# Kernel tuning notes

Measured on AMD Instinct MI355X. Metric: run time of the kernel, lower is better.

The kernel has to match this reference:

```python
import jax, jax.numpy as jnp
import numpy as np

INPUT_DIM = 128
HIDDEN_DIM = 128
N_PATIENTS = 200000
N_CONDITIONS = 5000
N_EDGES = 1000000
IN_FEAT = INPUT_DIM * 2 + 1  # 257


def _linear_params(key, fan_in, fan_out):
    # torch nn.Linear default init: U(-1/sqrt(fan_in), 1/sqrt(fan_in))
    kw, kb = jax.random.split(key)
    bound = 1.0 / np.sqrt(fan_in)
    W = jax.random.uniform(kw, (fan_in, fan_out), jnp.float32, -bound, bound)
    b = jax.random.uniform(kb, (fan_out,), jnp.float32, -bound, bound)
    return W, b


def setup_inputs() -> dict:
    key = jax.random.key(0)
    ks = jax.random.split(key, 8)
    patient_embeds = jax.random.normal(ks[0], (N_PATIENTS, INPUT_DIM), jnp.float32)
    condition_embeds = jax.random.normal(ks[1], (N_CONDITIONS, INPUT_DIM), jnp.float32)
    src_idx = jax.random.randint(ks[2], (N_EDGES,), 0, N_PATIENTS)
    dst_idx = jax.random.randint(ks[3], (N_EDGES,), 0, N_CONDITIONS)
    edge_index = jnp.stack([src_idx, dst_idx], axis=0)
    tte = jax.random.uniform(ks[4], (N_EDGES,), jnp.float32)
    W1, b1 = _linear_params(ks[5], IN_FEAT, HIDDEN_DIM)
    W2, b2 = _linear_params(ks[6], HIDDEN_DIM, HIDDEN_DIM)
    k7, k8 = jax.random.split(ks[7])
    Wo, bo = _linear_params(k7, HIDDEN_DIM, 1)
    Wr, br = _linear_params(k8, IN_FEAT, HIDDEN_DIM)
    return {
        "patient_embeds": patient_embeds,
        "condition_embeds": condition_embeds,
        "edge_index": edge_index,
        "tte": tte,
        "W1": W1, "b1": b1,
        "W2": W2, "b2": b2,
        "Wo": Wo, "bo": bo,
        "Wr": Wr, "br": br,
    }


def reference(patient_embeds, condition_embeds, edge_index, tte,
              W1, b1, W2, b2, Wo, bo, Wr, br):
    src = patient_embeds[edge_index[0]]        # [E, D]
    dst = condition_embeds[edge_index[1]]      # [E, D]
    x = jnp.concatenate([src, dst, tte[:, None]], axis=1)  # [E, 2D+1]
    h1 = jax.nn.relu(x @ W1 + b1)              # [E, H]
    res = x @ Wr + br                          # [E, H]
    h2 = jax.nn.relu(h1 @ W2 + b2 + res)       # [E, H]
    return (h2 @ Wo + bo).reshape(-1)          # [E]
```

## Files before the change

kernel.cpp:

```cpp
#include <hip/hip_runtime.h>
#include <hip/hip_bf16.h>

using u16   = unsigned short;
using u16x4 = __attribute__((ext_vector_type(4))) unsigned short;
using u16x8 = __attribute__((ext_vector_type(8))) unsigned short;
using s16x8 = __attribute__((ext_vector_type(8))) short;
using f32x4 = __attribute__((ext_vector_type(4))) float;

#define KPAD 136
#define XP   136
#define OP   264
#define EB   64

__device__ __forceinline__ float bf2f(u16 u){
  unsigned int x = ((unsigned int)u) << 16;
  float f; __builtin_memcpy(&f, &x, 4); return f;
}
__device__ __forceinline__ u16 f2bf(float f){
  __hip_bfloat16 h = __float2bfloat16(f);
  u16 u; __builtin_memcpy(&u, &h, 2); return u;
}
__device__ __forceinline__ f32x4 mfma16(s16x8 a, s16x8 b, f32x4 c){
  return __builtin_amdgcn_mfma_f32_16x16x32_bf16(a, b, c, 0, 0, 0);
}

__global__ __launch_bounds__(256) void prep_kernel(
    const float* __restrict__ W1, const float* __restrict__ W2,
    const float* __restrict__ Wo, const float* __restrict__ Wr,
    const float* __restrict__ b1, const float* __restrict__ b2,
    const float* __restrict__ br,
    u16* __restrict__ WF, u16* __restrict__ W2T, float* __restrict__ params)
{
  const int tid = blockIdx.x*256 + threadIdx.x;
  const int nth = gridDim.x*256;
  for (int id = tid; id < 131072; id += nth){
    const int j    = id & 7;
    const int lane = (id >> 3) & 63;
    const int pair = (id >> 9) & 1;
    const int ks   = (id >> 10) & 3;
    const int nb   = (id >> 12) & 15;
    const int h    = (id >> 16) & 1;
    const int k = ks*32 + (lane >> 4)*8 + j;
    const int n = nb*16 + (lane & 15);
    const float v = ((n < 128) ? W1 : Wr)[(h*128 + k)*128 + (n & 127)];
    const u16 hi = f2bf(v);
    WF[id] = pair ? f2bf(v - bf2f(hi)) : hi;
  }
  for (int id = tid; id < 128*128; id += nth){
    const int k = id >> 7, n = id & 127;
    W2T[n*KPAD + k] = f2bf(W2[k*128 + n]);
  }
  for (int id = tid; id < 128; id += nth){
    params[id]       = W1[256*128 + id];
    params[128 + id] = Wr[256*128 + id];
    params[256 + id] = Wo[id];
    params[384 + id]       = b1[id];
    params[384 + 128 + id] = br[id] + b2[id];
  }
}

__global__ __launch_bounds__(1024, 4) void mm_kernel(
    const float* __restrict__ emb, int nrows, int ntiles,
    const u16* __restrict__ WFh,
    const float* __restrict__ bias,
    u16* __restrict__ outbuf)
{
  __shared__ __align__(16) char smem_raw[2*128*XP*2];
  u16* xhi = (u16*)smem_raw;
  u16* xlo = xhi + 128*XP;
  u16* sO  = (u16*)smem_raw;
  const int t = threadIdx.x;
  const int l = t & 63, w = t >> 6;
  const int lrow = l & 15, lq = l >> 4;
  s16x8 wf0h, wf0l, wf1h, wf1l, wf2h, wf2l, wf3h, wf3l;
  {
    const u16* base = WFh + w*4096 + l*8;
    wf0h = *(const s16x8*)(base +    0); wf0l = *(const s16x8*)(base +  512);
    wf1h = *(const s16x8*)(base + 1024); wf1l = *(const s16x8*)(base + 1536);
    wf2h = *(const s16x8*)(base + 2048); wf2l = *(const s16x8*)(base + 2560);
    wf3h = *(const s16x8*)(base + 3072); wf3l = *(const s16x8*)(base + 3584);
  }
  float bv[4] = {0.f, 0.f, 0.f, 0.f};
  if (bias){
#pragma unroll
    for (int r = 0; r < 4; ++r) bv[r] = bias[w*16 + lq*4 + r];
  }
  for (int tile = blockIdx.x; tile < ntiles; tile += gridDim.x){
    const int row0 = tile*128;
    __syncthreads();
#pragma unroll
    for (int i = 0; i < 4; ++i){
      const int f4 = i*1024 + t;
      const int r = f4 >> 5, kc = f4 & 31;
      int grow = row0 + r; if (grow >= nrows) grow = nrows - 1;
      const float4 v = *(const float4*)(emb + (size_t)grow*128 + kc*4);
      const float vv[4] = {v.x, v.y, v.z, v.w};
      u16x4 h4, l4;
#pragma unroll
      for (int q = 0; q < 4; ++q){
        const u16 hi = f2bf(vv[q]);
        h4[q] = hi;
        l4[q] = f2bf(vv[q] - bf2f(hi));
      }
      *(u16x4*)(xhi + r*XP + kc*4) = h4;
      *(u16x4*)(xlo + r*XP + kc*4) = l4;
    }
    __syncthreads();
    f32x4 acc[8];
#pragma unroll
    for (int mb = 0; mb < 8; ++mb) acc[mb] = (f32x4){0.f,0.f,0.f,0.f};
#pragma unroll
    for (int mb = 0; mb < 8; ++mb){
      const int mro = (mb*16 + lrow)*XP + lq*8;
      const s16x8 xh0 = *(const s16x8*)(xhi + mro +  0);
      const s16x8 xl0 = *(const s16x8*)(xlo + mro +  0);
      const s16x8 xh1 = *(const s16x8*)(xhi + mro + 32);
      const s16x8 xl1 = *(const s16x8*)(xlo + mro + 32);
      const s16x8 xh2 = *(const s16x8*)(xhi + mro + 64);
      const s16x8 xl2 = *(const s16x8*)(xlo + mro + 64);
      const s16x8 xh3 = *(const s16x8*)(xhi + mro + 96);
      const s16x8 xl3 = *(const s16x8*)(xlo + mro + 96);
      acc[mb] = mfma16(wf0h, xh0, acc[mb]);
      acc[mb] = mfma16(wf0l, xh0, acc[mb]);
      acc[mb] = mfma16(wf0h, xl0, acc[mb]);
      acc[mb] = mfma16(wf1h, xh1, acc[mb]);
      acc[mb] = mfma16(wf1l, xh1, acc[mb]);
      acc[mb] = mfma16(wf1h, xl1, acc[mb]);
      acc[mb] = mfma16(wf2h, xh2, acc[mb]);
      acc[mb] = mfma16(wf2l, xh2, acc[mb]);
      acc[mb] = mfma16(wf2h, xl2, acc[mb]);
      acc[mb] = mfma16(wf3h, xh3, acc[mb]);
      acc[mb] = mfma16(wf3l, xh3, acc[mb]);
      acc[mb] = mfma16(wf3h, xl3, acc[mb]);
    }
    __syncthreads();
#pragma unroll
    for (int mb = 0; mb < 8; ++mb){
      const int m = mb*16 + lrow;
      u16x4 o;
#pragma unroll
      for (int r = 0; r < 4; ++r) o[r] = f2bf(acc[mb][r] + bv[r]);
      *(u16x4*)(sO + m*OP + w*16 + lq*4) = o;
    }
    __syncthreads();
#pragma unroll
    for (int i = 0; i < 4; ++i){
      const int idx = i*1024 + t;
      const int m = idx >> 5, c = idx & 31;
      const int grow = row0 + m;
      if (grow < nrows){
        const u16x8 v = *(const u16x8*)(sO + m*OP + c*8);
        *(u16x8*)(outbuf + (size_t)grow*256 + c*8) = v;
      }
    }
  }
}

__global__ __launch_bounds__(512, 4) void edge_kernel(
    const int* __restrict__ ei, const float* __restrict__ tte,
    const u16* __restrict__ PP, const u16* __restrict__ CC,
    const u16* __restrict__ W2T, const float* __restrict__ params,
    const float* __restrict__ bo_p, float* __restrict__ out, int E, int ntiles)
{
  __shared__ u16 sW2T[128*KPAD];
  __shared__ u16 sA[EB*KPAD];
  __shared__ u16 sR[EB*KPAD];
  __shared__ float sw1t[128], swrt[128], sWo[128];
  __shared__ int ssrc[EB], sdst[EB];
  __shared__ float stte[EB];
  __shared__ float souts[4][EB];
  const int t = threadIdx.x;
  {
    const u16x8* g = (const u16x8*)W2T;
    u16x8* s = (u16x8*)sW2T;
    for (int i = t; i < 128*KPAD/8; i += 512) s[i] = g[i];
  }
  if (t < 128){ sw1t[t] = params[t]; swrt[t] = params[128+t]; sWo[t] = params[256+t]; }
  const float bo = bo_p[0];
  const int l = t & 63, w = t >> 6;
  const int lrow = l & 15, lk = l >> 4;
  const int rh = w & 1, ch = w >> 1;

  for (int tile = blockIdx.x; tile < ntiles; tile += gridDim.x){
    const int e0 = tile * EB;
    if (t < EB){
      int e = e0 + t; if (e >= E) e = E - 1;
      ssrc[t] = ei[e]; sdst[t] = ei[E + e]; stte[t] = tte[e];
    }
    __syncthreads();
    u16x8 pv[4], cv[4];
#pragma unroll
    for (int i = 0; i < 4; ++i){
      const int id = i*512 + t;
      const int e = id >> 5, c = id & 31;
      pv[i] = *(const u16x8*)(PP + (size_t)ssrc[e]*256 + c*8);
      cv[i] = *(const u16x8*)(CC + (size_t)sdst[e]*256 + c*8);
    }
#pragma unroll
    for (int i = 0; i < 4; ++i){
      const int id = i*512 + t;
      const int e = id >> 5, c = id & 31;
      const float tt = stte[e];
      const int jj = (c & 15)*8;
      const float* wt = (c < 16) ? sw1t : swrt;
      u16x8 o;
#pragma unroll
      for (int q = 0; q < 8; ++q){
        float v = bf2f(pv[i][q]) + bf2f(cv[i][q]) + tt * wt[jj+q];
        if (c < 16) v = fmaxf(v, 0.f);
        o[q] = f2bf(v);
      }
      u16* dst = (c < 16) ? (sA + e*KPAD + jj) : (sR + e*KPAD + jj);
      *(u16x8*)dst = o;
    }
    __syncthreads();
    f32x4 acc[2][2];
#pragma unroll
    for (int mb = 0; mb < 2; ++mb)
#pragma unroll
      for (int nb = 0; nb < 2; ++nb) acc[mb][nb] = (f32x4){0.f,0.f,0.f,0.f};
#pragma unroll
    for (int ks = 0; ks < 4; ++ks){
      const int koff = ks*32 + lk*8;
      const s16x8 a0 = *(const s16x8*)(sA + (rh*32 + lrow)*KPAD + koff);
      const s16x8 a1 = *(const s16x8*)(sA + (rh*32 + 16 + lrow)*KPAD + koff);
      const s16x8 b0 = *(const s16x8*)(sW2T + (ch*32 + lrow)*KPAD + koff);
      const s16x8 b1 = *(const s16x8*)(sW2T + (ch*32 + 16 + lrow)*KPAD + koff);
      acc[0][0] = mfma16(a0, b0, acc[0][0]);
      acc[0][1] = mfma16(a0, b1, acc[0][1]);
      acc[1][0] = mfma16(a1, b0, acc[1][0]);
      acc[1][1] = mfma16(a1, b1, acc[1][1]);
    }
    float p[2][4] = {{0.f,0.f,0.f,0.f},{0.f,0.f,0.f,0.f}};
#pragma unroll
    for (int nb = 0; nb < 2; ++nb){
      const int col = ch*32 + nb*16 + lrow;
      const float wo = sWo[col];
#pragma unroll
      for (int mb = 0; mb < 2; ++mb){
#pragma unroll
        for (int r = 0; r < 4; ++r){
          const int row = rh*32 + mb*16 + lk*4 + r;
          float h2 = acc[mb][nb][r] + bf2f(sR[row*KPAD + col]);
          h2 = fmaxf(h2, 0.f);
          p[mb][r] += h2 * wo;
        }
      }
    }
#pragma unroll
    for (int off = 1; off < 16; off <<= 1){
#pragma unroll
      for (int mb = 0; mb < 2; ++mb)
#pragma unroll
        for (int r = 0; r < 4; ++r)
          p[mb][r] += __shfl_xor(p[mb][r], off, 64);
    }
    if (lrow == 0){
#pragma unroll
      for (int mb = 0; mb < 2; ++mb)
#pragma unroll
        for (int r = 0; r < 4; ++r)
          souts[ch][rh*32 + mb*16 + lk*4 + r] = p[mb][r];
    }
    __syncthreads();
    if (t < EB && e0 + t < E)
      out[e0 + t] = souts[0][t] + souts[1][t] + souts[2][t] + souts[3][t] + bo;
  }
}

__global__ __launch_bounds__(256) void fallback_kernel(
    const float* __restrict__ pe, const float* __restrict__ ce,
    const int* __restrict__ ei, const float* __restrict__ tte,
    const float* __restrict__ W1, const float* __restrict__ b1,
    const float* __restrict__ W2, const float* __restrict__ b2,
    const float* __restrict__ Wo, const float* __restrict__ bo,
    const float* __restrict__ Wr, const float* __restrict__ br,
    float* __restrict__ out, int E)
{
  __shared__ float sh1[4][128];
  const int w = threadIdx.x >> 6, l = threadIdx.x & 63;
  const int e_raw = blockIdx.x*4 + w;
  const int e = e_raw < E ? e_raw : E-1;
  const int s = ei[e], d = ei[E + e];
  const float tt = tte[e];
  const float* xs = pe + (size_t)s*128;
  const float* xd = ce + (size_t)d*128;
  const float x0 = xs[l], x1 = xs[64+l], x2 = xd[l], x3 = xd[64+l];
  float h1a = b1[l], h1b = b1[64+l];
  float ra = br[l], rb = br[64+l];
  for (int k = 0; k < 256; ++k){
    const float xv = (k < 64) ? x0 : (k < 128) ? x1 : (k < 192) ? x2 : x3;
    const float xk = __shfl(xv, k & 63, 64);
    h1a += xk * W1[k*128 + l];
    h1b += xk * W1[k*128 + 64 + l];
    ra  += xk * Wr[k*128 + l];
    rb  += xk * Wr[k*128 + 64 + l];
  }
  h1a += tt * W1[256*128 + l];  h1b += tt * W1[256*128 + 64 + l];
  ra  += tt * Wr[256*128 + l];  rb  += tt * Wr[256*128 + 64 + l];
  sh1[w][l] = fmaxf(h1a, 0.f);
  sh1[w][64+l] = fmaxf(h1b, 0.f);
  __syncthreads();
  float h2a = b2[l] + ra, h2b = b2[64+l] + rb;
  for (int k = 0; k < 128; ++k){
    const float hk = sh1[w][k];
    h2a += hk * W2[k*128 + l];
    h2b += hk * W2[k*128 + 64 + l];
  }
  float sum = fmaxf(h2a,0.f)*Wo[l] + fmaxf(h2b,0.f)*Wo[64+l];
  for (int off = 1; off < 64; off <<= 1) sum += __shfl_xor(sum, off, 64);
  if (l == 0 && e_raw < E) out[e_raw] = sum + bo[0];
}

extern "C" void kernel_launch(void* const* d_in, const int* in_sizes, int n_in,
                              void* d_out, int out_size, void* d_ws, size_t ws_size,
                              hipStream_t stream)
{
  const float* pe  = (const float*)d_in[0];
  const float* ce  = (const float*)d_in[1];
  const int*   ei  = (const int*)d_in[2];
  const float* tte = (const float*)d_in[3];
  const float* W1  = (const float*)d_in[4];
  const float* b1  = (const float*)d_in[5];
  const float* W2  = (const float*)d_in[6];
  const float* b2  = (const float*)d_in[7];
  const float* Wo  = (const float*)d_in[8];
  const float* bo  = (const float*)d_in[9];
  const float* Wr  = (const float*)d_in[10];
  const float* br  = (const float*)d_in[11];
  float* out = (float*)d_out;
  const int E = in_sizes[3];
  const int npat  = in_sizes[0] / 128;
  const int ncond = in_sizes[1] / 128;

  char* ws = (char*)d_ws;
  const size_t sz_PP  = (size_t)npat  * 256 * 2;
  const size_t sz_CC  = (size_t)ncond * 256 * 2;
  const size_t sz_WF  = (size_t)131072 * 2;
  const size_t sz_W2T = (size_t)128 * KPAD * 2;
  const size_t off_PP = 0;
  const size_t off_CC = off_PP + sz_PP;
  const size_t off_WF = off_CC + sz_CC;
  const size_t off_W2T = off_WF + sz_WF;
  const size_t off_params = off_W2T + sz_W2T;
  const size_t ws_needed = off_params + 640*4;

  if (ws_size >= ws_needed){
    u16* PP     = (u16*)(ws + off_PP);
    u16* CCb    = (u16*)(ws + off_CC);
    u16* WF     = (u16*)(ws + off_WF);
    u16* W2T    = (u16*)(ws + off_W2T);
    float* params = (float*)(ws + off_params);
    prep_kernel<<<64, 256, 0, stream>>>(W1, W2, Wo, Wr, b1, b2, br, WF, W2T, params);
    const int ptiles = (npat + 127)/128;
    mm_kernel<<<512, 1024, 0, stream>>>(pe, npat, ptiles, WF, nullptr, PP);
    const int ctiles = (ncond + 127)/128;
    mm_kernel<<<ctiles, 1024, 0, stream>>>(ce, ncond, ctiles, WF + 65536, params + 384, CCb);
    const int etiles = (E + EB - 1)/EB;
    edge_kernel<<<512, 512, 0, stream>>>(ei, tte, PP, CCb, W2T, params, bo, out, E, etiles);
  } else {
    fallback_kernel<<<(E + 3)/4, 256, 0, stream>>>(pe, ce, ei, tte, W1, b1, W2, b2, Wo, bo, Wr, br, out, E);
  }
}
```

Baseline: 381.8 us.

## Prefetch next edge tile gathers, keep W2 fragments in registers, shrink mm tiles

```diff
diff --git a/kernel.cpp b/kernel.cpp
--- a/kernel.cpp
+++ b/kernel.cpp
@@ -12,6 +12,8 @@
 #define OP   264
 #define EB   64
 
+#define BARRIER() asm volatile("s_waitcnt lgkmcnt(0)\n\ts_barrier" ::: "memory")
+
 __device__ __forceinline__ float bf2f(u16 u){
   unsigned int x = ((unsigned int)u) << 16;
   float f; __builtin_memcpy(&f, &x, 4); return f;
@@ -29,7 +31,7 @@
     const float* __restrict__ Wo, const float* __restrict__ Wr,
     const float* __restrict__ b1, const float* __restrict__ b2,
     const float* __restrict__ br,
-    u16* __restrict__ WF, u16* __restrict__ W2T, float* __restrict__ params)
+    u16* __restrict__ WF, u16* __restrict__ WF2, float* __restrict__ params)
 {
   const int tid = blockIdx.x*256 + threadIdx.x;
   const int nth = gridDim.x*256;
@@ -46,9 +48,14 @@
     const u16 hi = f2bf(v);
     WF[id] = pair ? f2bf(v - bf2f(hi)) : hi;
   }
-  for (int id = tid; id < 128*128; id += nth){
-    const int k = id >> 7, n = id & 127;
-    W2T[n*KPAD + k] = f2bf(W2[k*128 + n]);
+  for (int id = tid; id < 16384; id += nth){
+    const int j    = id & 7;
+    const int lane = (id >> 3) & 63;
+    const int ks   = (id >> 9) & 3;
+    const int nb   = (id >> 11) & 7;
+    const int k = ks*32 + (lane >> 4)*8 + j;
+    const int n = nb*16 + (lane & 15);
+    WF2[id] = f2bf(W2[k*128 + n]);
   }
   for (int id = tid; id < 128; id += nth){
     params[id]       = W1[256*128 + id];
@@ -59,38 +66,42 @@
   }
 }
 
-__global__ __launch_bounds__(1024, 4) void mm_kernel(
+__global__ __launch_bounds__(512, 8) void mm_kernel(
     const float* __restrict__ emb, int nrows, int ntiles,
-    const u16* __restrict__ WFh,
-    const float* __restrict__ bias,
+    const u16* __restrict__ WFh, const float* __restrict__ bias,
     u16* __restrict__ outbuf)
 {
-  __shared__ __align__(16) char smem_raw[2*128*XP*2];
+  __shared__ __align__(16) char smem_raw[64*XP*2*2];
   u16* xhi = (u16*)smem_raw;
-  u16* xlo = xhi + 128*XP;
+  u16* xlo = xhi + 64*XP;
   u16* sO  = (u16*)smem_raw;
   const int t = threadIdx.x;
   const int l = t & 63, w = t >> 6;
   const int lrow = l & 15, lq = l >> 4;
-  s16x8 wf0h, wf0l, wf1h, wf1l, wf2h, wf2l, wf3h, wf3l;
-  {
-    const u16* base = WFh + w*4096 + l*8;
-    wf0h = *(const s16x8*)(base +    0); wf0l = *(const s16x8*)(base +  512);
-    wf1h = *(const s16x8*)(base + 1024); wf1l = *(const s16x8*)(base + 1536);
-    wf2h = *(const s16x8*)(base + 2048); wf2l = *(const s16x8*)(base + 2560);
-    wf3h = *(const s16x8*)(base + 3072); wf3l = *(const s16x8*)(base + 3584);
-  }
-  float bv[4] = {0.f, 0.f, 0.f, 0.f};
+  s16x8 wf[2][4][2];
+#pragma unroll
+  for (int nbh = 0; nbh < 2; ++nbh)
+#pragma unroll
+    for (int ks = 0; ks < 4; ++ks){
+      const int nb = w + nbh*8;
+      const u16* base = WFh + (size_t)((nb*4 + ks)*2)*512 + l*8;
+      wf[nbh][ks][0] = *(const s16x8*)(base);
+      wf[nbh][ks][1] = *(const s16x8*)(base + 512);
+    }
+  float bv[2][4] = {{0.f,0.f,0.f,0.f},{0.f,0.f,0.f,0.f}};
   if (bias){
 #pragma unroll
-    for (int r = 0; r < 4; ++r) bv[r] = bias[w*16 + lq*4 + r];
+    for (int nbh = 0; nbh < 2; ++nbh)
+#pragma unroll
+      for (int r = 0; r < 4; ++r)
+        bv[nbh][r] = bias[(w + nbh*8)*16 + lq*4 + r];
   }
   for (int tile = blockIdx.x; tile < ntiles; tile += gridDim.x){
-    const int row0 = tile*128;
-    __syncthreads();
-#pragma unroll
-    for (int i = 0; i < 4; ++i){
-      const int f4 = i*1024 + t;
+    const int row0 = tile*64;
+    BARRIER();
+#pragma unroll
+    for (int i = 0; i < 4; ++i){
+      const int f4 = i*512 + t;
       const int r = f4 >> 5, kc = f4 & 31;
       int grow = row0 + r; if (grow >= nrows) grow = nrows - 1;
       const float4 v = *(const float4*)(emb + (size_t)grow*128 + kc*4);
@@ -105,47 +116,42 @@
       *(u16x4*)(xhi + r*XP + kc*4) = h4;
       *(u16x4*)(xlo + r*XP + kc*4) = l4;
     }
-    __syncthreads();
-    f32x4 acc[8];
-#pragma unroll
-    for (int mb = 0; mb < 8; ++mb) acc[mb] = (f32x4){0.f,0.f,0.f,0.f};
-#pragma unroll
-    for (int mb = 0; mb < 8; ++mb){
+    BARRIER();
+    f32x4 acc[2][4];
+#pragma unroll
+    for (int a = 0; a < 2; ++a)
+#pragma unroll
+      for (int b = 0; b < 4; ++b) acc[a][b] = (f32x4){0.f,0.f,0.f,0.f};
+#pragma unroll
+    for (int mb = 0; mb < 4; ++mb){
       const int mro = (mb*16 + lrow)*XP + lq*8;
-      const s16x8 xh0 = *(const s16x8*)(xhi + mro +  0);
-      const s16x8 xl0 = *(const s16x8*)(xlo + mro +  0);
-      const s16x8 xh1 = *(const s16x8*)(xhi + mro + 32);
-      const s16x8 xl1 = *(const s16x8*)(xlo + mro + 32);
-      const s16x8 xh2 = *(const s16x8*)(xhi + mro + 64);
-      const s16x8 xl2 = *(const s16x8*)(xlo + mro + 64);
-      const s16x8 xh3 = *(const s16x8*)(xhi + mro + 96);
-      const s16x8 xl3 = *(const s16x8*)(xlo + mro + 96);
-      acc[mb] = mfma16(wf0h, xh0, acc[mb]);
-      acc[mb] = mfma16(wf0l, xh0, acc[mb]);
-      acc[mb] = mfma16(wf0h, xl0, acc[mb]);
-      acc[mb] = mfma16(wf1h, xh1, acc[mb]);
-      acc[mb] = mfma16(wf1l, xh1, acc[mb]);
-      acc[mb] = mfma16(wf1h, xl1, acc[mb]);
-      acc[mb] = mfma16(wf2h, xh2, acc[mb]);
-      acc[mb] = mfma16(wf2l, xh2, acc[mb]);
-      acc[mb] = mfma16(wf2h, xl2, acc[mb]);
-      acc[mb] = mfma16(wf3h, xh3, acc[mb]);
-      acc[mb] = mfma16(wf3l, xh3, acc[mb]);
-      acc[mb] = mfma16(wf3h, xl3, acc[mb]);
-    }
-    __syncthreads();
-#pragma unroll
-    for (int mb = 0; mb < 8; ++mb){
-      const int m = mb*16 + lrow;
-      u16x4 o;
-#pragma unroll
-      for (int r = 0; r < 4; ++r) o[r] = f2bf(acc[mb][r] + bv[r]);
-      *(u16x4*)(sO + m*OP + w*16 + lq*4) = o;
-    }
-    __syncthreads();
-#pragma unroll
-    for (int i = 0; i < 4; ++i){
-      const int idx = i*1024 + t;
+#pragma unroll
+      for (int ks = 0; ks < 4; ++ks){
+        const s16x8 xh = *(const s16x8*)(xhi + mro + ks*32);
+        const s16x8 xl = *(const s16x8*)(xlo + mro + ks*32);
+#pragma unroll
+        for (int nbh = 0; nbh < 2; ++nbh){
+          acc[nbh][mb] = mfma16(wf[nbh][ks][0], xh, acc[nbh][mb]);
+          acc[nbh][mb] = mfma16(wf[nbh][ks][1], xh, acc[nbh][mb]);
+          acc[nbh][mb] = mfma16(wf[nbh][ks][0], xl, acc[nbh][mb]);
+        }
+      }
+    }
+    BARRIER();
+#pragma unroll
+    for (int nbh = 0; nbh < 2; ++nbh)
+#pragma unroll
+      for (int mb = 0; mb < 4; ++mb){
+        const int m = mb*16 + lrow;
+        u16x4 o;
+#pragma unroll
+        for (int r = 0; r < 4; ++r) o[r] = f2bf(acc[nbh][mb][r] + bv[nbh][r]);
+        *(u16x4*)(sO + m*OP + (w + nbh*8)*16 + lq*4) = o;
+      }
+    BARRIER();
+#pragma unroll
+    for (int i = 0; i < 4; ++i){
+      const int idx = i*512 + t;
       const int m = idx >> 5, c = idx & 31;
       const int grow = row0 + m;
       if (grow < nrows){
@@ -156,115 +162,136 @@
   }
 }
 
-__global__ __launch_bounds__(512, 4) void edge_kernel(
+__global__ __launch_bounds__(512, 8) void edge_kernel(
     const int* __restrict__ ei, const float* __restrict__ tte,
     const u16* __restrict__ PP, const u16* __restrict__ CC,
-    const u16* __restrict__ W2T, const float* __restrict__ params,
+    const u16* __restrict__ WF2, const float* __restrict__ params,
     const float* __restrict__ bo_p, float* __restrict__ out, int E, int ntiles)
 {
-  __shared__ u16 sW2T[128*KPAD];
   __shared__ u16 sA[EB*KPAD];
   __shared__ u16 sR[EB*KPAD];
-  __shared__ float sw1t[128], swrt[128], sWo[128];
-  __shared__ int ssrc[EB], sdst[EB];
-  __shared__ float stte[EB];
   __shared__ float souts[4][EB];
   const int t = threadIdx.x;
-  {
-    const u16x8* g = (const u16x8*)W2T;
-    u16x8* s = (u16x8*)sW2T;
-    for (int i = t; i < 128*KPAD/8; i += 512) s[i] = g[i];
-  }
-  if (t < 128){ sw1t[t] = params[t]; swrt[t] = params[128+t]; sWo[t] = params[256+t]; }
-  const float bo = bo_p[0];
   const int l = t & 63, w = t >> 6;
   const int lrow = l & 15, lk = l >> 4;
   const int rh = w & 1, ch = w >> 1;
-
-  for (int tile = blockIdx.x; tile < ntiles; tile += gridDim.x){
-    const int e0 = tile * EB;
-    if (t < EB){
-      int e = e0 + t; if (e >= E) e = E - 1;
-      ssrc[t] = ei[e]; sdst[t] = ei[E + e]; stte[t] = tte[e];
-    }
-    __syncthreads();
-    u16x8 pv[4], cv[4];
-#pragma unroll
-    for (int i = 0; i < 4; ++i){
-      const int id = i*512 + t;
-      const int e = id >> 5, c = id & 31;
-      pv[i] = *(const u16x8*)(PP + (size_t)ssrc[e]*256 + c*8);
-      cv[i] = *(const u16x8*)(CC + (size_t)sdst[e]*256 + c*8);
-    }
-#pragma unroll
-    for (int i = 0; i < 4; ++i){
-      const int id = i*512 + t;
-      const int e = id >> 5, c = id & 31;
-      const float tt = stte[e];
-      const int jj = (c & 15)*8;
-      const float* wt = (c < 16) ? sw1t : swrt;
+  const int gid = t >> 5, gl = t & 31;
+  const float bo = bo_p[0];
+  s16x8 wf2[2][4];
+#pragma unroll
+  for (int nb = 0; nb < 2; ++nb)
+#pragma unroll
+    for (int ks = 0; ks < 4; ++ks)
+      wf2[nb][ks] = *(const s16x8*)(WF2 + (size_t)(((ch*2 + nb)*4 + ks)*64 + l)*8);
+  float wt[8];
+  {
+    const float* base = params + ((gl < 16) ? 0 : 128) + (gl & 15)*8;
+#pragma unroll
+    for (int q = 0; q < 8; ++q) wt[q] = base[q];
+  }
+  float wo[2][4];
+#pragma unroll
+  for (int nb = 0; nb < 2; ++nb){
+    const float4 v = *(const float4*)(params + 256 + ch*32 + nb*16 + lk*4);
+    wo[nb][0] = v.x; wo[nb][1] = v.y; wo[nb][2] = v.z; wo[nb][3] = v.w;
+  }
+
+  int tile = blockIdx.x;
+  if (tile >= ntiles) return;
+  float ctt[4];
+  u16x8 cpv[4], ccv[4];
+  {
+    int cs[4], cd[4];
+#pragma unroll
+    for (int i = 0; i < 4; ++i){
+      int e = tile*EB + i*16 + gid; if (e >= E) e = E - 1;
+      cs[i] = ei[e]; cd[i] = ei[E + e]; ctt[i] = tte[e];
+    }
+#pragma unroll
+    for (int i = 0; i < 4; ++i){
+      cpv[i] = *(const u16x8*)(PP + (size_t)cs[i]*256 + gl*8);
+      ccv[i] = *(const u16x8*)(CC + (size_t)cd[i]*256 + gl*8);
+    }
+  }
+
+  for (; tile < ntiles; tile += gridDim.x){
+    const int ntile = tile + gridDim.x;
+    int nxs[4], nxd[4]; float ntt[4];
+#pragma unroll
+    for (int i = 0; i < 4; ++i){
+      int e = ntile*EB + i*16 + gid; if (e >= E) e = E - 1;
+      nxs[i] = ei[e]; nxd[i] = ei[E + e]; ntt[i] = tte[e];
+    }
+    BARRIER();
+#pragma unroll
+    for (int i = 0; i < 4; ++i){
+      const int e = i*16 + gid;
+      const int jj = (gl & 15)*8;
+      const float tt = ctt[i];
       u16x8 o;
 #pragma unroll
       for (int q = 0; q < 8; ++q){
-        float v = bf2f(pv[i][q]) + bf2f(cv[i][q]) + tt * wt[jj+q];
-        if (c < 16) v = fmaxf(v, 0.f);
+        float v = bf2f(cpv[i][q]) + bf2f(ccv[i][q]) + tt * wt[q];
+        if (gl < 16) v = fmaxf(v, 0.f);
         o[q] = f2bf(v);
       }
-      u16* dst = (c < 16) ? (sA + e*KPAD + jj) : (sR + e*KPAD + jj);
+      u16* dst = (gl < 16) ? (sA + e*KPAD + jj) : (sR + e*KPAD + jj);
       *(u16x8*)dst = o;
     }
-    __syncthreads();
+    u16x8 npv[4], ncv[4];
+#pragma unroll
+    for (int i = 0; i < 4; ++i){
+      npv[i] = *(const u16x8*)(PP + (size_t)nxs[i]*256 + gl*8);
+      ncv[i] = *(const u16x8*)(CC + (size_t)nxd[i]*256 + gl*8);
+    }
+    BARRIER();
     f32x4 acc[2][2];
 #pragma unroll
-    for (int mb = 0; mb < 2; ++mb)
-#pragma unroll
-      for (int nb = 0; nb < 2; ++nb) acc[mb][nb] = (f32x4){0.f,0.f,0.f,0.f};
+    for (int a = 0; a < 2; ++a)
+#pragma unroll
+      for (int b = 0; b < 2; ++b) acc[a][b] = (f32x4){0.f,0.f,0.f,0.f};
 #pragma unroll
     for (int ks = 0; ks < 4; ++ks){
       const int koff = ks*32 + lk*8;
-      const s16x8 a0 = *(const s16x8*)(sA + (rh*32 + lrow)*KPAD + koff);
-      const s16x8 a1 = *(const s16x8*)(sA + (rh*32 + 16 + lrow)*KPAD + koff);
-      const s16x8 b0 = *(const s16x8*)(sW2T + (ch*32 + lrow)*KPAD + koff);
-      const s16x8 b1 = *(const s16x8*)(sW2T + (ch*32 + 16 + lrow)*KPAD + koff);
-      acc[0][0] = mfma16(a0, b0, acc[0][0]);
-      acc[0][1] = mfma16(a0, b1, acc[0][1]);
-      acc[1][0] = mfma16(a1, b0, acc[1][0]);
-      acc[1][1] = mfma16(a1, b1, acc[1][1]);
-    }
-    float p[2][4] = {{0.f,0.f,0.f,0.f},{0.f,0.f,0.f,0.f}};
-#pragma unroll
-    for (int nb = 0; nb < 2; ++nb){
-      const int col = ch*32 + nb*16 + lrow;
-      const float wo = sWo[col];
-#pragma unroll
-      for (int mb = 0; mb < 2; ++mb){
+      const s16x8 h0 = *(const s16x8*)(sA + (rh*32 + lrow)*KPAD + koff);
+      const s16x8 h1 = *(const s16x8*)(sA + (rh*32 + 16 + lrow)*KPAD + koff);
+      acc[0][0] = mfma16(wf2[0][ks], h0, acc[0][0]);
+      acc[0][1] = mfma16(wf2[0][ks], h1, acc[0][1]);
+      acc[1][0] = mfma16(wf2[1][ks], h0, acc[1][0]);
+      acc[1][1] = mfma16(wf2[1][ks], h1, acc[1][1]);
+    }
+    float p[2] = {0.f, 0.f};
+#pragma unroll
+    for (int mb = 0; mb < 2; ++mb){
+      const int edge = rh*32 + mb*16 + lrow;
+#pragma unroll
+      for (int nb = 0; nb < 2; ++nb){
+        const int col0 = ch*32 + nb*16 + lk*4;
+        const u16x4 rv = *(const u16x4*)(sR + edge*KPAD + col0);
 #pragma unroll
         for (int r = 0; r < 4; ++r){
-          const int row = rh*32 + mb*16 + lk*4 + r;
-          float h2 = acc[mb][nb][r] + bf2f(sR[row*KPAD + col]);
+          float h2 = acc[nb][mb][r] + bf2f(rv[r]);
           h2 = fmaxf(h2, 0.f);
-          p[mb][r] += h2 * wo;
+          p[mb] += h2 * wo[nb][r];
         }
       }
-    }
-#pragma unroll
-    for (int off = 1; off < 16; off <<= 1){
-#pragma unroll
-      for (int mb = 0; mb < 2; ++mb)
-#pragma unroll
-        for (int r = 0; r < 4; ++r)
-          p[mb][r] += __shfl_xor(p[mb][r], off, 64);
-    }
-    if (lrow == 0){
-#pragma unroll
-      for (int mb = 0; mb < 2; ++mb)
-#pragma unroll
-        for (int r = 0; r < 4; ++r)
-          souts[ch][rh*32 + mb*16 + lk*4 + r] = p[mb][r];
-    }
-    __syncthreads();
-    if (t < EB && e0 + t < E)
-      out[e0 + t] = souts[0][t] + souts[1][t] + souts[2][t] + souts[3][t] + bo;
+      p[mb] += __shfl_xor(p[mb], 16, 64);
+      p[mb] += __shfl_xor(p[mb], 32, 64);
+    }
+    if (lk == 0){
+      souts[ch][rh*32 + lrow]      = p[0];
+      souts[ch][rh*32 + 16 + lrow] = p[1];
+    }
+    BARRIER();
+    if (t < EB){
+      const int eo = tile*EB + t;
+      if (eo < E)
+        out[eo] = souts[0][t] + souts[1][t] + souts[2][t] + souts[3][t] + bo;
+    }
+#pragma unroll
+    for (int i = 0; i < 4; ++i){
+      ctt[i] = ntt[i]; cpv[i] = npv[i]; ccv[i] = ncv[i];
+    }
   }
 }
 
@@ -337,27 +364,27 @@
   const size_t sz_PP  = (size_t)npat  * 256 * 2;
   const size_t sz_CC  = (size_t)ncond * 256 * 2;
   const size_t sz_WF  = (size_t)131072 * 2;
-  const size_t sz_W2T = (size_t)128 * KPAD * 2;
-  const size_t off_PP = 0;
-  const size_t off_CC = off_PP + sz_PP;
-  const size_t off_WF = off_CC + sz_CC;
-  const size_t off_W2T = off_WF + sz_WF;
-  const size_t off_params = off_W2T + sz_W2T;
+  const size_t sz_WF2 = (size_t)16384 * 2;
+  const size_t off_PP  = 0;
+  const size_t off_CC  = off_PP + sz_PP;
+  const size_t off_WF  = off_CC + sz_CC;
+  const size_t off_WF2 = off_WF + sz_WF;
+  const size_t off_params = off_WF2 + sz_WF2;
   const size_t ws_needed = off_params + 640*4;
 
   if (ws_size >= ws_needed){
     u16* PP     = (u16*)(ws + off_PP);
     u16* CCb    = (u16*)(ws + off_CC);
     u16* WF     = (u16*)(ws + off_WF);
-    u16* W2T    = (u16*)(ws + off_W2T);
+    u16* WF2    = (u16*)(ws + off_WF2);
     float* params = (float*)(ws + off_params);
-    prep_kernel<<<64, 256, 0, stream>>>(W1, W2, Wo, Wr, b1, b2, br, WF, W2T, params);
-    const int ptiles = (npat + 127)/128;
-    mm_kernel<<<512, 1024, 0, stream>>>(pe, npat, ptiles, WF, nullptr, PP);
-    const int ctiles = (ncond + 127)/128;
-    mm_kernel<<<ctiles, 1024, 0, stream>>>(ce, ncond, ctiles, WF + 65536, params + 384, CCb);
+    prep_kernel<<<64, 256, 0, stream>>>(W1, W2, Wo, Wr, b1, b2, br, WF, WF2, params);
+    const int ptiles = (npat + 63)/64;
+    mm_kernel<<<(ptiles < 1024 ? ptiles : 1024), 512, 0, stream>>>(pe, npat, ptiles, WF, nullptr, PP);
+    const int ctiles = (ncond + 63)/64;
+    mm_kernel<<<(ctiles < 1024 ? ctiles : 1024), 512, 0, stream>>>(ce, ncond, ctiles, WF + 65536, params + 384, CCb);
     const int etiles = (E + EB - 1)/EB;
-    edge_kernel<<<512, 512, 0, stream>>>(ei, tte, PP, CCb, W2T, params, bo, out, E, etiles);
+    edge_kernel<<<(etiles < 1024 ? etiles : 1024), 512, 0, stream>>>(ei, tte, PP, CCb, WF2, params, bo, out, E, etiles);
   } else {
     fallback_kernel<<<(E + 3)/4, 256, 0, stream>>>(pe, ce, ei, tte, W1, b1, W2, b2, Wo, bo, Wr, br, out, E);
   }
```

Measured after the change: 961.3 us. 2.52x slower.
